# Kernel optimization log

Hardware: AMD Instinct MI355X
Metric: run time of the kernel (lower is better)

The kernel has to match this reference:

```python
import jax, jax.numpy as jnp
import numpy as np

DN = ('NHWC', 'HWIO', 'NHWC')
BN_EPS = 1e-3  # Keras BatchNormalization default


def _conv(x, w, pad):
    return jax.lax.conv_general_dilated(x, w, (1, 1), pad, dimension_numbers=DN)


def _bn(x, p):
    # p: [4, C] rows = (gamma, beta, moving_mean, moving_var), inference mode
    g, b, m, v = p[0], p[1], p[2], p[3]
    return g * (x - m) * jax.lax.rsqrt(v + BN_EPS) + b


def _hard_swish(x):
    return x * jnp.clip(x + 3.0, 0.0, 6.0) * (1.0 / 6.0)


def _conv_block(x, w, bn_p, pad):
    # Conv module: ZeroPad+Conv2D(no bias) -> BN -> hard_swish
    return _hard_swish(_bn(_conv(x, w, pad), bn_p))


def setup_inputs() -> dict:
    key = jax.random.key(0)
    ks = jax.random.split(key, 17)
    s = 0.05  # keep activations numerically tame
    inp = {
        'x': jax.random.normal(ks[0], (16, 160, 160, 128), jnp.float32),
        'cv1_w': jax.random.normal(ks[1], (1, 1, 128, 64), jnp.float32) * s,
        'cv1_bn': jax.random.uniform(ks[2], (4, 64), jnp.float32),
        'm0_cv1_w': jax.random.normal(ks[3], (1, 1, 64, 64), jnp.float32) * s,
        'm0_cv1_bn': jax.random.uniform(ks[4], (4, 64), jnp.float32),
        'm0_cv2_w': jax.random.normal(ks[5], (3, 3, 64, 64), jnp.float32) * s,
        'm0_cv2_bn': jax.random.uniform(ks[6], (4, 64), jnp.float32),
        'm1_cv1_w': jax.random.normal(ks[7], (1, 1, 64, 64), jnp.float32) * s,
        'm1_cv1_bn': jax.random.uniform(ks[8], (4, 64), jnp.float32),
        'm1_cv2_w': jax.random.normal(ks[9], (3, 3, 64, 64), jnp.float32) * s,
        'm1_cv2_bn': jax.random.uniform(ks[10], (4, 64), jnp.float32),
        'cv3_w': jax.random.normal(ks[11], (1, 1, 64, 64), jnp.float32) * s,
        'cv2p_w': jax.random.normal(ks[12], (1, 1, 128, 64), jnp.float32) * s,
        'bn_cat': jax.random.uniform(ks[13], (4, 128), jnp.float32),
        'cv4_w': jax.random.normal(ks[14], (1, 1, 128, 128), jnp.float32) * s,
        'cv4_bn': jax.random.uniform(ks[15], (4, 128), jnp.float32),
    }
    return inp


def reference(x, cv1_w, cv1_bn, m0_cv1_w, m0_cv1_bn, m0_cv2_w, m0_cv2_bn,
              m1_cv1_w, m1_cv1_bn, m1_cv2_w, m1_cv2_bn,
              cv3_w, cv2p_w, bn_cat, cv4_w, cv4_bn):
    # BottleneckCSP(filters=128, n=2, shortcut=True, expansion=0.5)
    y = _conv_block(x, cv1_w, cv1_bn, 'VALID')            # cv1: 1x1 -> mid=64
    # m: 2 standard Bottlenecks(mid, mid, shortcut=True, expansion=1.0)
    for w1, p1, w2, p2 in ((m0_cv1_w, m0_cv1_bn, m0_cv2_w, m0_cv2_bn),
                           (m1_cv1_w, m1_cv1_bn, m1_cv2_w, m1_cv2_bn)):
        h = _conv_block(y, w1, p1, 'VALID')               # 1x1
        h = _conv_block(h, w2, p2, 'SAME')                # 3x3 (pad=1)
        y = y + h                                         # residual add
    x1 = _conv(y, cv3_w, 'VALID')                         # plain 1x1 conv, no BN/act
    x2 = _conv(x, cv2p_w, 'VALID')                        # plain 1x1 conv on input
    xc = jnp.concatenate([x1, x2], axis=-1)               # [B,H,W,128]
    xc = _bn(xc, bn_cat)
    xc = jnp.where(xc >= 0, xc, 0.1 * xc)                 # LeakyReLU(0.1)
    out = _conv_block(xc, cv4_w, cv4_bn, 'VALID')         # cv4: 1x1 -> 128
    return out
```

## Files before the change

### kernel.cpp

```cpp
#include <hip/hip_runtime.h>
#include <hip/hip_bf16.h>

using bf16   = __bf16;
using bf16x8 = __attribute__((ext_vector_type(8))) __bf16;
using bf16x4 = __attribute__((ext_vector_type(4))) __bf16;
using f32x4  = __attribute__((ext_vector_type(4))) float;

#define MFMA16(W, X, C) __builtin_amdgcn_mfma_f32_16x16x32_bf16((W), (X), (C), 0, 0, 0)

__device__ __forceinline__ float hsw(float x) {
    return x * fminf(fmaxf(x + 3.f, 0.f), 6.f) * (1.f / 6.f);
}
__device__ __forceinline__ float lrelu(float x) {
    return x >= 0.f ? x : 0.1f * x;
}
__device__ __forceinline__ bf16x8 zero8() {
    bf16x8 t;
#pragma unroll
    for (int b = 0; b < 8; ++b) t[b] = (bf16)0.f;
    return t;
}
__device__ __forceinline__ f32x4 zero4f() {
    f32x4 t = {0.f, 0.f, 0.f, 0.f};
    return t;
}

template <int KTOT, int COUT>
__device__ void fill_w(bf16* dst, const float* __restrict__ W, int tid) {
    constexpr int NKS = KTOT / 32, NCT = COUT / 16;
    for (int idx = tid; idx < NKS * NCT * 64; idx += 256) {
        int lane = idx & 63;
        int f = idx >> 6;
        int ct = f % NCT, ks = f / NCT;
        int j = ct * 16 + (lane & 15);
        int kb = ks * 32 + ((lane >> 4) << 3);
        bf16* d = dst + (size_t)idx * 8;
#pragma unroll
        for (int b = 0; b < 8; ++b) d[b] = (bf16)W[(size_t)(kb + b) * COUT + j];
    }
}

__device__ void fill_bn_(float* sc, float* sh, const float* __restrict__ p,
                         int C, int off, int n, int tid) {
    for (int c = tid; c < n; c += 256) {
        float g = p[off + c], b = p[C + off + c];
        float m = p[2 * C + off + c], v = p[3 * C + off + c];
        float s = g * rsqrtf(v + 1e-3f);
        sc[c] = s;
        sh[c] = b - m * s;
    }
}

__global__ __launch_bounds__(256) void k_head(
    const float* __restrict__ x, const float* __restrict__ w1,
    const float* __restrict__ bn1, const float* __restrict__ w2p,
    const float* __restrict__ bncat, bf16* __restrict__ y, bf16* __restrict__ x2) {
    __shared__ bf16 wa[128 * 64], wb[128 * 64];
    __shared__ float sca[64], sha[64], scb[64], shb[64];
    int tid = threadIdx.x;
    fill_w<128, 64>(wa, w1, tid);
    fill_w<128, 64>(wb, w2p, tid);
    fill_bn_(sca, sha, bn1, 64, 0, 64, tid);
    fill_bn_(scb, shb, bncat, 128, 64, 64, tid);
    __syncthreads();
    int lane = tid & 63, wid = tid >> 6;
    int lr = lane & 15, lg = lane >> 4;
    int m0 = blockIdx.x * 128 + wid * 32;

    f32x4 accy[2][4], accx[2][4];
#pragma unroll
    for (int rt = 0; rt < 2; ++rt)
#pragma unroll
        for (int ct = 0; ct < 4; ++ct) { accy[rt][ct] = zero4f(); accx[rt][ct] = zero4f(); }

#pragma unroll
    for (int ks = 0; ks < 4; ++ks) {
        bf16x8 xa[2];
#pragma unroll
        for (int rt = 0; rt < 2; ++rt) {
            const float* p = x + (size_t)(m0 + rt * 16 + lr) * 128 + ks * 32 + lg * 8;
            f32x4 v0 = *(const f32x4*)p;
            f32x4 v1 = *(const f32x4*)(p + 4);
            bf16x8 t;
#pragma unroll
            for (int b = 0; b < 4; ++b) { t[b] = (bf16)v0[b]; t[b + 4] = (bf16)v1[b]; }
            xa[rt] = t;
        }
#pragma unroll
        for (int ct = 0; ct < 4; ++ct) {
            bf16x8 fa = *(const bf16x8*)(wa + (size_t)((ks * 4 + ct) * 64 + lane) * 8);
            bf16x8 fb = *(const bf16x8*)(wb + (size_t)((ks * 4 + ct) * 64 + lane) * 8);
#pragma unroll
            for (int rt = 0; rt < 2; ++rt) {
                accy[rt][ct] = MFMA16(fa, xa[rt], accy[rt][ct]);
                accx[rt][ct] = MFMA16(fb, xa[rt], accx[rt][ct]);
            }
        }
    }
#pragma unroll
    for (int rt = 0; rt < 2; ++rt) {
        size_t r = (size_t)(m0 + rt * 16 + lr);
#pragma unroll
        for (int ct = 0; ct < 4; ++ct) {
            int j0 = ct * 16 + lg * 4;
            f32x4 s4 = *(const f32x4*)(sca + j0), h4 = *(const f32x4*)(sha + j0);
            f32x4 a = accy[rt][ct];
            bf16x4 oy, ox;
#pragma unroll
            for (int b = 0; b < 4; ++b) oy[b] = (bf16)hsw(a[b] * s4[b] + h4[b]);
            *(bf16x4*)(y + r * 64 + j0) = oy;
            s4 = *(const f32x4*)(scb + j0);
            h4 = *(const f32x4*)(shb + j0);
            a = accx[rt][ct];
#pragma unroll
            for (int b = 0; b < 4; ++b) ox[b] = (bf16)lrelu(a[b] * s4[b] + h4[b]);
            *(bf16x4*)(x2 + r * 64 + j0) = ox;
        }
    }
}

__global__ __launch_bounds__(256) void k_cb64(
    const bf16* __restrict__ in, const float* __restrict__ W,
    const float* __restrict__ bnp, bf16* __restrict__ out) {
    __shared__ bf16 wl[64 * 64];
    __shared__ float sc[64], sh[64];
    int tid = threadIdx.x;
    fill_w<64, 64>(wl, W, tid);
    fill_bn_(sc, sh, bnp, 64, 0, 64, tid);
    __syncthreads();
    int lane = tid & 63, wid = tid >> 6;
    int lr = lane & 15, lg = lane >> 4;
    bf16x8 wf[2][4];
#pragma unroll
    for (int ks = 0; ks < 2; ++ks)
#pragma unroll
        for (int ct = 0; ct < 4; ++ct)
            wf[ks][ct] = *(const bf16x8*)(wl + (size_t)((ks * 4 + ct) * 64 + lane) * 8);

    int m0 = blockIdx.x * 256 + wid * 64;
    f32x4 acc[4][4];
#pragma unroll
    for (int rt = 0; rt < 4; ++rt)
#pragma unroll
        for (int ct = 0; ct < 4; ++ct) acc[rt][ct] = zero4f();

#pragma unroll
    for (int ks = 0; ks < 2; ++ks) {
        bf16x8 xa[4];
#pragma unroll
        for (int rt = 0; rt < 4; ++rt)
            xa[rt] = *(const bf16x8*)(in + (size_t)(m0 + rt * 16 + lr) * 64 + ks * 32 + lg * 8);
#pragma unroll
        for (int ct = 0; ct < 4; ++ct)
#pragma unroll
            for (int rt = 0; rt < 4; ++rt)
                acc[rt][ct] = MFMA16(wf[ks][ct], xa[rt], acc[rt][ct]);
    }
#pragma unroll
    for (int rt = 0; rt < 4; ++rt) {
        size_t r = (size_t)(m0 + rt * 16 + lr);
#pragma unroll
        for (int ct = 0; ct < 4; ++ct) {
            int j0 = ct * 16 + lg * 4;
            f32x4 s4 = *(const f32x4*)(sc + j0), h4 = *(const f32x4*)(sh + j0);
            f32x4 a = acc[rt][ct];
            bf16x4 o;
#pragma unroll
            for (int b = 0; b < 4; ++b) o[b] = (bf16)hsw(a[b] * s4[b] + h4[b]);
            *(bf16x4*)(out + r * 64 + j0) = o;
        }
    }
}

__global__ __launch_bounds__(256) void k_c3(
    const bf16* __restrict__ in, const float* __restrict__ W,
    const float* __restrict__ bnp, bf16* __restrict__ y) {
    __shared__ bf16 wl[576 * 64];
    __shared__ float sc[64], sh[64];
    int tid = threadIdx.x;
    fill_w<576, 64>(wl, W, tid);
    fill_bn_(sc, sh, bnp, 64, 0, 64, tid);
    __syncthreads();
    int lane = tid & 63, wid = tid >> 6;
    int lr = lane & 15, lg = lane >> 4;
    int m0 = blockIdx.x * 256 + wid * 64;

    int row[4], wc[4], hr[4];
#pragma unroll
    for (int rt = 0; rt < 4; ++rt) {
        int r = m0 + rt * 16 + lr;
        row[rt] = r;
        int q = r / 160;
        wc[rt] = r - q * 160;
        hr[rt] = q % 160;
    }
    f32x4 acc[4][4];
#pragma unroll
    for (int rt = 0; rt < 4; ++rt)
#pragma unroll
        for (int ct = 0; ct < 4; ++ct) acc[rt][ct] = zero4f();

#pragma unroll
    for (int tap = 0; tap < 9; ++tap) {
        const int dy = tap / 3 - 1, dx = tap % 3 - 1;
        const int roff = dy * 160 + dx;
#pragma unroll
        for (int ks2 = 0; ks2 < 2; ++ks2) {
            int ks = tap * 2 + ks2;
            bf16x8 xa[4];
#pragma unroll
            for (int rt = 0; rt < 4; ++rt) {
                bool v = ((unsigned)(hr[rt] + dy) < 160u) && ((unsigned)(wc[rt] + dx) < 160u);
                bf16x8 t = zero8();
                if (v)
                    t = *(const bf16x8*)(in + (size_t)(row[rt] + roff) * 64 + ks2 * 32 + lg * 8);
                xa[rt] = t;
            }
            bf16x8 wfr[4];
#pragma unroll
            for (int ct = 0; ct < 4; ++ct)
                wfr[ct] = *(const bf16x8*)(wl + (size_t)((ks * 4 + ct) * 64 + lane) * 8);
#pragma unroll
            for (int ct = 0; ct < 4; ++ct)
#pragma unroll
                for (int rt = 0; rt < 4; ++rt)
                    acc[rt][ct] = MFMA16(wfr[ct], xa[rt], acc[rt][ct]);
        }
    }
#pragma unroll
    for (int rt = 0; rt < 4; ++rt) {
        size_t r = (size_t)row[rt];
#pragma unroll
        for (int ct = 0; ct < 4; ++ct) {
            int j0 = ct * 16 + lg * 4;
            f32x4 s4 = *(const f32x4*)(sc + j0), h4 = *(const f32x4*)(sh + j0);
            f32x4 a = acc[rt][ct];
            bf16x4 old = *(const bf16x4*)(y + r * 64 + j0);
            bf16x4 o;
#pragma unroll
            for (int b = 0; b < 4; ++b)
                o[b] = (bf16)((float)old[b] + hsw(a[b] * s4[b] + h4[b]));
            *(bf16x4*)(y + r * 64 + j0) = o;
        }
    }
}

__global__ __launch_bounds__(256) void k_tail(
    const bf16* __restrict__ y, const bf16* __restrict__ x2,
    const float* __restrict__ w3, const float* __restrict__ w4,
    const float* __restrict__ bncat, const float* __restrict__ bn4,
    float* __restrict__ out) {
    __shared__ bf16 w3l[64 * 64];
    __shared__ bf16 w4l[128 * 128];
    __shared__ float sc1[64], sh1[64], sc4[128], sh4[128];
    __shared__ bf16 tl[4 * 32 * 64];
    int tid = threadIdx.x;
    fill_w<64, 64>(w3l, w3, tid);
    fill_w<128, 128>(w4l, w4, tid);
    fill_bn_(sc1, sh1, bncat, 128, 0, 64, tid);
    fill_bn_(sc4, sh4, bn4, 128, 0, 128, tid);
    __syncthreads();
    int lane = tid & 63, wid = tid >> 6;
    int lr = lane & 15, lg = lane >> 4;
    int m0 = blockIdx.x * 128 + wid * 32;
    char* tlw = (char*)(tl + (size_t)wid * 32 * 64);

    f32x4 a1[2][4];
#pragma unroll
    for (int rt = 0; rt < 2; ++rt)
#pragma unroll
        for (int ct = 0; ct < 4; ++ct) a1[rt][ct] = zero4f();
#pragma unroll
    for (int ks = 0; ks < 2; ++ks) {
        bf16x8 xa[2];
#pragma unroll
        for (int rt = 0; rt < 2; ++rt)
            xa[rt] = *(const bf16x8*)(y + (size_t)(m0 + rt * 16 + lr) * 64 + ks * 32 + lg * 8);
#pragma unroll
        for (int ct = 0; ct < 4; ++ct) {
            bf16x8 wfr = *(const bf16x8*)(w3l + (size_t)((ks * 4 + ct) * 64 + lane) * 8);
#pragma unroll
            for (int rt = 0; rt < 2; ++rt) a1[rt][ct] = MFMA16(wfr, xa[rt], a1[rt][ct]);
        }
    }
#pragma unroll
    for (int rt = 0; rt < 2; ++rt) {
        int rr = rt * 16 + lr;
#pragma unroll
        for (int ct = 0; ct < 4; ++ct) {
            int j0 = ct * 16 + lg * 4;
            f32x4 s4 = *(const f32x4*)(sc1 + j0), h4 = *(const f32x4*)(sh1 + j0);
            f32x4 a = a1[rt][ct];
            bf16x4 o;
#pragma unroll
            for (int b = 0; b < 4; ++b) o[b] = (bf16)lrelu(a[b] * s4[b] + h4[b]);
            int byo = (rr * 128 + j0 * 2) ^ ((rr & 7) << 4);
            *(bf16x4*)(tlw + byo) = o;
        }
    }
    __syncthreads();

    f32x4 a2[2][8];
#pragma unroll
    for (int rt = 0; rt < 2; ++rt)
#pragma unroll
        for (int ct = 0; ct < 8; ++ct) a2[rt][ct] = zero4f();
#pragma unroll
    for (int ks = 0; ks < 4; ++ks) {
        bf16x8 xa[2];
        if (ks < 2) {
#pragma unroll
            for (int rt = 0; rt < 2; ++rt) {
                int rr = rt * 16 + lr;
                int byo = (rr * 128 + (ks * 32 + lg * 8) * 2) ^ ((rr & 7) << 4);
                xa[rt] = *(const bf16x8*)(tlw + byo);
            }
        } else {
#pragma unroll
            for (int rt = 0; rt < 2; ++rt)
                xa[rt] = *(const bf16x8*)(x2 + (size_t)(m0 + rt * 16 + lr) * 64 +
                                          (ks - 2) * 32 + lg * 8);
        }
#pragma unroll
        for (int ct = 0; ct < 8; ++ct) {
            bf16x8 wfr = *(const bf16x8*)(w4l + (size_t)((ks * 8 + ct) * 64 + lane) * 8);
#pragma unroll
            for (int rt = 0; rt < 2; ++rt) a2[rt][ct] = MFMA16(wfr, xa[rt], a2[rt][ct]);
        }
    }
#pragma unroll
    for (int rt = 0; rt < 2; ++rt) {
        size_t r = (size_t)(m0 + rt * 16 + lr);
#pragma unroll
        for (int ct = 0; ct < 8; ++ct) {
            int j0 = ct * 16 + lg * 4;
            f32x4 s4 = *(const f32x4*)(sc4 + j0), h4 = *(const f32x4*)(sh4 + j0);
            f32x4 a = a2[rt][ct];
            f32x4 o;
#pragma unroll
            for (int b = 0; b < 4; ++b) o[b] = hsw(a[b] * s4[b] + h4[b]);
            *(f32x4*)(out + r * 128 + j0) = o;
        }
    }
}

extern "C" void kernel_launch(void* const* d_in, const int* in_sizes, int n_in,
                              void* d_out, int out_size, void* d_ws, size_t ws_size,
                              hipStream_t stream) {
    const float* x      = (const float*)d_in[0];
    const float* cv1_w  = (const float*)d_in[1];
    const float* cv1_bn = (const float*)d_in[2];
    const float* m0c1w  = (const float*)d_in[3];
    const float* m0c1b  = (const float*)d_in[4];
    const float* m0c2w  = (const float*)d_in[5];
    const float* m0c2b  = (const float*)d_in[6];
    const float* m1c1w  = (const float*)d_in[7];
    const float* m1c1b  = (const float*)d_in[8];
    const float* m1c2w  = (const float*)d_in[9];
    const float* m1c2b  = (const float*)d_in[10];
    const float* cv3_w  = (const float*)d_in[11];
    const float* cv2p_w = (const float*)d_in[12];
    const float* bn_cat = (const float*)d_in[13];
    const float* cv4_w  = (const float*)d_in[14];
    const float* cv4_bn = (const float*)d_in[15];
    float* out = (float*)d_out;

    const size_t M = (size_t)16 * 160 * 160;
    bf16* y  = (bf16*)d_ws;
    bf16* x2 = y + M * 64;
    bf16* h  = x2 + M * 64;

    dim3 blk(256);
    k_head<<<dim3((int)(M / 128)), blk, 0, stream>>>(x, cv1_w, cv1_bn, cv2p_w, bn_cat, y, x2);
    k_cb64<<<dim3((int)(M / 256)), blk, 0, stream>>>(y, m0c1w, m0c1b, h);
    k_c3 <<<dim3((int)(M / 256)), blk, 0, stream>>>(h, m0c2w, m0c2b, y);
    k_cb64<<<dim3((int)(M / 256)), blk, 0, stream>>>(y, m1c1w, m1c1b, h);
    k_c3 <<<dim3((int)(M / 256)), blk, 0, stream>>>(h, m1c2w, m1c2b, y);
    k_tail<<<dim3((int)(M / 128)), blk, 0, stream>>>(y, x2, cv3_w, cv4_w, bn_cat, cv4_bn, out);
}
```

Baseline: 729.2 us.

## Pre-pack weights and BN params once in a prep kernel, read from global

Adds a small prep kernel that converts all conv weights into the MFMA fragment layout in bf16 and folds the BN parameters into scale/shift, writing both to workspace. The main kernels drop their per-block LDS weight fills and __syncthreads and load weight fragments straight from global memory, relying on cache hits. Occupancy hints are also added to the launch bounds. This removes redundant per-block conversion work and LDS pressure, but makes weight reads in the inner loop of the 3x3 conv go through the cache hierarchy instead of LDS.

```diff
diff --git a/kernel.cpp b/kernel.cpp
--- a/kernel.cpp
+++ b/kernel.cpp
@@ -8,6 +8,17 @@
 
 #define MFMA16(W, X, C) __builtin_amdgcn_mfma_f32_16x16x32_bf16((W), (X), (C), 0, 0, 0)
 
+static constexpr size_t M_TOT = (size_t)16 * 160 * 160;
+
+static constexpr size_t O_CV1  = 0;
+static constexpr size_t O_CV2P = 8192;
+static constexpr size_t O_M0C1 = 16384;
+static constexpr size_t O_M0C2 = 20480;
+static constexpr size_t O_M1C1 = 57344;
+static constexpr size_t O_M1C2 = 61440;
+static constexpr size_t O_CV3  = 98304;
+static constexpr size_t O_CV4  = 102400;
+
 __device__ __forceinline__ float hsw(float x) {
     return x * fminf(fmaxf(x + 3.f, 0.f), 6.f) * (1.f / 6.f);
 }
@@ -26,43 +37,67 @@
 }
 
 template <int KTOT, int COUT>
-__device__ void fill_w(bf16* dst, const float* __restrict__ W, int tid) {
+__device__ void prep_w(bf16* __restrict__ dst, const float* __restrict__ W,
+                       int gid, int gs) {
     constexpr int NKS = KTOT / 32, NCT = COUT / 16;
-    for (int idx = tid; idx < NKS * NCT * 64; idx += 256) {
+    for (int idx = gid; idx < NKS * NCT * 64; idx += gs) {
         int lane = idx & 63;
         int f = idx >> 6;
         int ct = f % NCT, ks = f / NCT;
         int j = ct * 16 + (lane & 15);
         int kb = ks * 32 + ((lane >> 4) << 3);
-        bf16* d = dst + (size_t)idx * 8;
-#pragma unroll
-        for (int b = 0; b < 8; ++b) d[b] = (bf16)W[(size_t)(kb + b) * COUT + j];
-    }
-}
-
-__device__ void fill_bn_(float* sc, float* sh, const float* __restrict__ p,
-                         int C, int off, int n, int tid) {
-    for (int c = tid; c < n; c += 256) {
+        bf16x8 t;
+#pragma unroll
+        for (int b = 0; b < 8; ++b) t[b] = (bf16)W[(size_t)(kb + b) * COUT + j];
+        *(bf16x8*)(dst + (size_t)idx * 8) = t;
+    }
+}
+
+__device__ void prep_bn(float* __restrict__ dst, const float* __restrict__ p,
+                        int C, int off, int n, int gid, int gs) {
+    for (int c = gid; c < n; c += gs) {
         float g = p[off + c], b = p[C + off + c];
         float m = p[2 * C + off + c], v = p[3 * C + off + c];
         float s = g * rsqrtf(v + 1e-3f);
-        sc[c] = s;
-        sh[c] = b - m * s;
-    }
-}
-
-__global__ __launch_bounds__(256) void k_head(
-    const float* __restrict__ x, const float* __restrict__ w1,
-    const float* __restrict__ bn1, const float* __restrict__ w2p,
-    const float* __restrict__ bncat, bf16* __restrict__ y, bf16* __restrict__ x2) {
-    __shared__ bf16 wa[128 * 64], wb[128 * 64];
-    __shared__ float sca[64], sha[64], scb[64], shb[64];
+        dst[c] = s;
+        dst[128 + c] = b - m * s;
+    }
+}
+
+__global__ __launch_bounds__(256) void k_prep(
+    const float* __restrict__ w1, const float* __restrict__ w2p,
+    const float* __restrict__ m0c1w, const float* __restrict__ m0c2w,
+    const float* __restrict__ m1c1w, const float* __restrict__ m1c2w,
+    const float* __restrict__ cv3w, const float* __restrict__ cv4w,
+    const float* __restrict__ bn1, const float* __restrict__ bncat,
+    const float* __restrict__ m0c1b, const float* __restrict__ m0c2b,
+    const float* __restrict__ m1c1b, const float* __restrict__ m1c2b,
+    const float* __restrict__ bn4, bf16* __restrict__ wb, float* __restrict__ bnb) {
+    int gid = blockIdx.x * 256 + threadIdx.x;
+    int gs = gridDim.x * 256;
+    prep_w<128, 64>(wb + O_CV1, w1, gid, gs);
+    prep_w<128, 64>(wb + O_CV2P, w2p, gid, gs);
+    prep_w<64, 64>(wb + O_M0C1, m0c1w, gid, gs);
+    prep_w<576, 64>(wb + O_M0C2, m0c2w, gid, gs);
+    prep_w<64, 64>(wb + O_M1C1, m1c1w, gid, gs);
+    prep_w<576, 64>(wb + O_M1C2, m1c2w, gid, gs);
+    prep_w<64, 64>(wb + O_CV3, cv3w, gid, gs);
+    prep_w<128, 128>(wb + O_CV4, cv4w, gid, gs);
+    prep_bn(bnb + 0 * 256, bn1, 64, 0, 64, gid, gs);
+    prep_bn(bnb + 1 * 256, bncat, 128, 64, 64, gid, gs);
+    prep_bn(bnb + 2 * 256, m0c1b, 64, 0, 64, gid, gs);
+    prep_bn(bnb + 3 * 256, m0c2b, 64, 0, 64, gid, gs);
+    prep_bn(bnb + 4 * 256, m1c1b, 64, 0, 64, gid, gs);
+    prep_bn(bnb + 5 * 256, m1c2b, 64, 0, 64, gid, gs);
+    prep_bn(bnb + 6 * 256, bncat, 128, 0, 64, gid, gs);
+    prep_bn(bnb + 7 * 256, bn4, 128, 0, 128, gid, gs);
+}
+
+__global__ __launch_bounds__(256, 3) void k_head(
+    const float* __restrict__ x, const bf16* __restrict__ wa,
+    const bf16* __restrict__ wbq, const float* __restrict__ bna,
+    const float* __restrict__ bnb, bf16* __restrict__ y, bf16* __restrict__ x2) {
     int tid = threadIdx.x;
-    fill_w<128, 64>(wa, w1, tid);
-    fill_w<128, 64>(wb, w2p, tid);
-    fill_bn_(sca, sha, bn1, 64, 0, 64, tid);
-    fill_bn_(scb, shb, bncat, 128, 64, 64, tid);
-    __syncthreads();
     int lane = tid & 63, wid = tid >> 6;
     int lr = lane & 15, lg = lane >> 4;
     int m0 = blockIdx.x * 128 + wid * 32;
@@ -89,7 +124,7 @@
 #pragma unroll
         for (int ct = 0; ct < 4; ++ct) {
             bf16x8 fa = *(const bf16x8*)(wa + (size_t)((ks * 4 + ct) * 64 + lane) * 8);
-            bf16x8 fb = *(const bf16x8*)(wb + (size_t)((ks * 4 + ct) * 64 + lane) * 8);
+            bf16x8 fb = *(const bf16x8*)(wbq + (size_t)((ks * 4 + ct) * 64 + lane) * 8);
 #pragma unroll
             for (int rt = 0; rt < 2; ++rt) {
                 accy[rt][ct] = MFMA16(fa, xa[rt], accy[rt][ct]);
@@ -103,14 +138,14 @@
 #pragma unroll
         for (int ct = 0; ct < 4; ++ct) {
             int j0 = ct * 16 + lg * 4;
-            f32x4 s4 = *(const f32x4*)(sca + j0), h4 = *(const f32x4*)(sha + j0);
+            f32x4 s4 = *(const f32x4*)(bna + j0), h4 = *(const f32x4*)(bna + 128 + j0);
             f32x4 a = accy[rt][ct];
             bf16x4 oy, ox;
 #pragma unroll
             for (int b = 0; b < 4; ++b) oy[b] = (bf16)hsw(a[b] * s4[b] + h4[b]);
             *(bf16x4*)(y + r * 64 + j0) = oy;
-            s4 = *(const f32x4*)(scb + j0);
-            h4 = *(const f32x4*)(shb + j0);
+            s4 = *(const f32x4*)(bnb + j0);
+            h4 = *(const f32x4*)(bnb + 128 + j0);
             a = accx[rt][ct];
 #pragma unroll
             for (int b = 0; b < 4; ++b) ox[b] = (bf16)lrelu(a[b] * s4[b] + h4[b]);
@@ -119,15 +154,10 @@
     }
 }
 
-__global__ __launch_bounds__(256) void k_cb64(
-    const bf16* __restrict__ in, const float* __restrict__ W,
+__global__ __launch_bounds__(256, 4) void k_cb64(
+    const bf16* __restrict__ in, const bf16* __restrict__ wg,
     const float* __restrict__ bnp, bf16* __restrict__ out) {
-    __shared__ bf16 wl[64 * 64];
-    __shared__ float sc[64], sh[64];
     int tid = threadIdx.x;
-    fill_w<64, 64>(wl, W, tid);
-    fill_bn_(sc, sh, bnp, 64, 0, 64, tid);
-    __syncthreads();
     int lane = tid & 63, wid = tid >> 6;
     int lr = lane & 15, lg = lane >> 4;
     bf16x8 wf[2][4];
@@ -135,7 +165,7 @@
     for (int ks = 0; ks < 2; ++ks)
 #pragma unroll
         for (int ct = 0; ct < 4; ++ct)
-            wf[ks][ct] = *(const bf16x8*)(wl + (size_t)((ks * 4 + ct) * 64 + lane) * 8);
+            wf[ks][ct] = *(const bf16x8*)(wg + (size_t)((ks * 4 + ct) * 64 + lane) * 8);
 
     int m0 = blockIdx.x * 256 + wid * 64;
     f32x4 acc[4][4];
@@ -162,7 +192,7 @@
 #pragma unroll
         for (int ct = 0; ct < 4; ++ct) {
             int j0 = ct * 16 + lg * 4;
-            f32x4 s4 = *(const f32x4*)(sc + j0), h4 = *(const f32x4*)(sh + j0);
+            f32x4 s4 = *(const f32x4*)(bnp + j0), h4 = *(const f32x4*)(bnp + 128 + j0);
             f32x4 a = acc[rt][ct];
             bf16x4 o;
 #pragma unroll
@@ -172,18 +202,13 @@
     }
 }
 
-__global__ __launch_bounds__(256) void k_c3(
-    const bf16* __restrict__ in, const float* __restrict__ W,
+__global__ __launch_bounds__(256, 3) void k_c3(
+    const bf16* __restrict__ in, const bf16* __restrict__ wg,
     const float* __restrict__ bnp, bf16* __restrict__ y) {
-    __shared__ bf16 wl[576 * 64];
-    __shared__ float sc[64], sh[64];
     int tid = threadIdx.x;
-    fill_w<576, 64>(wl, W, tid);
-    fill_bn_(sc, sh, bnp, 64, 0, 64, tid);
-    __syncthreads();
-    int lane = tid & 63, wid = tid >> 6;
+    int lane = tid & 63;
     int lr = lane & 15, lg = lane >> 4;
-    int m0 = blockIdx.x * 256 + wid * 64;
+    int m0 = blockIdx.x * 256 + (tid >> 6) * 64;
 
     int row[4], wc[4], hr[4];
 #pragma unroll
@@ -199,6 +224,8 @@
     for (int rt = 0; rt < 4; ++rt)
 #pragma unroll
         for (int ct = 0; ct < 4; ++ct) acc[rt][ct] = zero4f();
+
+    const bf16* wl = wg + (size_t)lane * 8;
 
 #pragma unroll
     for (int tap = 0; tap < 9; ++tap) {
@@ -219,7 +246,7 @@
             bf16x8 wfr[4];
 #pragma unroll
             for (int ct = 0; ct < 4; ++ct)
-                wfr[ct] = *(const bf16x8*)(wl + (size_t)((ks * 4 + ct) * 64 + lane) * 8);
+                wfr[ct] = *(const bf16x8*)(wl + (size_t)((ks * 4 + ct) * 64) * 8);
 #pragma unroll
             for (int ct = 0; ct < 4; ++ct)
 #pragma unroll
@@ -233,7 +260,7 @@
 #pragma unroll
         for (int ct = 0; ct < 4; ++ct) {
             int j0 = ct * 16 + lg * 4;
-            f32x4 s4 = *(const f32x4*)(sc + j0), h4 = *(const f32x4*)(sh + j0);
+            f32x4 s4 = *(const f32x4*)(bnp + j0), h4 = *(const f32x4*)(bnp + 128 + j0);
             f32x4 a = acc[rt][ct];
             bf16x4 old = *(const bf16x4*)(y + r * 64 + j0);
             bf16x4 o;
@@ -245,21 +272,13 @@
     }
 }
 
-__global__ __launch_bounds__(256) void k_tail(
+__global__ __launch_bounds__(256, 3) void k_tail(
     const bf16* __restrict__ y, const bf16* __restrict__ x2,
-    const float* __restrict__ w3, const float* __restrict__ w4,
-    const float* __restrict__ bncat, const float* __restrict__ bn4,
+    const bf16* __restrict__ w3g, const bf16* __restrict__ w4g,
+    const float* __restrict__ bnlo, const float* __restrict__ bn4,
     float* __restrict__ out) {
-    __shared__ bf16 w3l[64 * 64];
-    __shared__ bf16 w4l[128 * 128];
-    __shared__ float sc1[64], sh1[64], sc4[128], sh4[128];
     __shared__ bf16 tl[4 * 32 * 64];
     int tid = threadIdx.x;
-    fill_w<64, 64>(w3l, w3, tid);
-    fill_w<128, 128>(w4l, w4, tid);
-    fill_bn_(sc1, sh1, bncat, 128, 0, 64, tid);
-    fill_bn_(sc4, sh4, bn4, 128, 0, 128, tid);
-    __syncthreads();
     int lane = tid & 63, wid = tid >> 6;
     int lr = lane & 15, lg = lane >> 4;
     int m0 = blockIdx.x * 128 + wid * 32;
@@ -278,7 +297,7 @@
             xa[rt] = *(const bf16x8*)(y + (size_t)(m0 + rt * 16 + lr) * 64 + ks * 32 + lg * 8);
 #pragma unroll
         for (int ct = 0; ct < 4; ++ct) {
-            bf16x8 wfr = *(const bf16x8*)(w3l + (size_t)((ks * 4 + ct) * 64 + lane) * 8);
+            bf16x8 wfr = *(const bf16x8*)(w3g + (size_t)((ks * 4 + ct) * 64 + lane) * 8);
 #pragma unroll
             for (int rt = 0; rt < 2; ++rt) a1[rt][ct] = MFMA16(wfr, xa[rt], a1[rt][ct]);
         }
@@ -289,7 +308,7 @@
 #pragma unroll
         for (int ct = 0; ct < 4; ++ct) {
             int j0 = ct * 16 + lg * 4;
-            f32x4 s4 = *(const f32x4*)(sc1 + j0), h4 = *(const f32x4*)(sh1 + j0);
+            f32x4 s4 = *(const f32x4*)(bnlo + j0), h4 = *(const f32x4*)(bnlo + 128 + j0);
             f32x4 a = a1[rt][ct];
             bf16x4 o;
 #pragma unroll
@@ -323,7 +342,7 @@
         }
 #pragma unroll
         for (int ct = 0; ct < 8; ++ct) {
-            bf16x8 wfr = *(const bf16x8*)(w4l + (size_t)((ks * 8 + ct) * 64 + lane) * 8);
+            bf16x8 wfr = *(const bf16x8*)(w4g + (size_t)((ks * 8 + ct) * 64 + lane) * 8);
 #pragma unroll
             for (int rt = 0; rt < 2; ++rt) a2[rt][ct] = MFMA16(wfr, xa[rt], a2[rt][ct]);
         }
@@ -334,7 +353,7 @@
 #pragma unroll
         for (int ct = 0; ct < 8; ++ct) {
             int j0 = ct * 16 + lg * 4;
-            f32x4 s4 = *(const f32x4*)(sc4 + j0), h4 = *(const f32x4*)(sh4 + j0);
+            f32x4 s4 = *(const f32x4*)(bn4 + j0), h4 = *(const f32x4*)(bn4 + 128 + j0);
             f32x4 a = a2[rt][ct];
             f32x4 o;
 #pragma unroll
@@ -365,16 +384,23 @@
     const float* cv4_bn = (const float*)d_in[15];
     float* out = (float*)d_out;
 
-    const size_t M = (size_t)16 * 160 * 160;
+    const size_t M = M_TOT;
     bf16* y  = (bf16*)d_ws;
     bf16* x2 = y + M * 64;
     bf16* h  = x2 + M * 64;
+    bf16* wb = h + M * 64;
+    float* bnb = (float*)(wb + 120832);
 
     dim3 blk(256);
-    k_head<<<dim3((int)(M / 128)), blk, 0, stream>>>(x, cv1_w, cv1_bn, cv2p_w, bn_cat, y, x2);
-    k_cb64<<<dim3((int)(M / 256)), blk, 0, stream>>>(y, m0c1w, m0c1b, h);
-    k_c3 <<<dim3((int)(M / 256)), blk, 0, stream>>>(h, m0c2w, m0c2b, y);
-    k_cb64<<<dim3((int)(M / 256)), blk, 0, stream>>>(y, m1c1w, m1c1b, h);
-    k_c3 <<<dim3((int)(M / 256)), blk, 0, stream>>>(h, m1c2w, m1c2b, y);
-    k_tail<<<dim3((int)(M / 128)), blk, 0, stream>>>(y, x2, cv3_w, cv4_w, bn_cat, cv4_bn, out);
-}
+    k_prep<<<dim3(64), blk, 0, stream>>>(cv1_w, cv2p_w, m0c1w, m0c2w, m1c1w, m1c2w,
+                                         cv3_w, cv4_w, cv1_bn, bn_cat, m0c1b, m0c2b,
+                                         m1c1b, m1c2b, cv4_bn, wb, bnb);
+    k_head<<<dim3((int)(M / 128)), blk, 0, stream>>>(
+        x, wb + O_CV1, wb + O_CV2P, bnb + 0 * 256, bnb + 1 * 256, y, x2);
+    k_cb64<<<dim3((int)(M / 256)), blk, 0, stream>>>(y, wb + O_M0C1, bnb + 2 * 256, h);
+    k_c3 <<<dim3((int)(M / 256)), blk, 0, stream>>>(h, wb + O_M0C2, bnb + 3 * 256, y);
+    k_cb64<<<dim3((int)(M / 256)), blk, 0, stream>>>(y, wb + O_M1C1, bnb + 4 * 256, h);
+    k_c3 <<<dim3((int)(M / 256)), blk, 0, stream>>>(h, wb + O_M1C2, bnb + 5 * 256, y);
+    k_tail<<<dim3((int)(M / 128)), blk, 0, stream>>>(
+        y, x2, wb + O_CV3, wb + O_CV4, bnb + 6 * 256, bnb + 7 * 256, out);
+}
```

After: 753.8 us. +3.4%, slower.
